# Kernel optimization log

Measured on AMD Instinct MI355X. Metric: run time of the kernel, lower is better.

Reference implementation:

```python
import jax, jax.numpy as jnp
import numpy as np

EMBED = 1024
HEADS = 16
HEAD_DIM = EMBED // HEADS
SCALE = HEAD_DIM ** -0.5


def setup_inputs() -> dict:
    key = jax.random.key(0)
    ks = jax.random.split(key, 5)
    B, N = 2, 2048
    x = jax.random.normal(ks[0], (B, N, EMBED), dtype=jnp.float32)
    # qkv Linear: weight [3*EMBED, EMBED], bias [3*EMBED]
    w_qkv = jax.random.normal(ks[1], (3 * EMBED, EMBED), dtype=jnp.float32) * (EMBED ** -0.5)
    b_qkv = jnp.zeros((3 * EMBED,), dtype=jnp.float32)
    # proj Linear: weight [EMBED, EMBED], bias [EMBED]
    w_proj = jax.random.normal(ks[2], (EMBED, EMBED), dtype=jnp.float32) * (EMBED ** -0.5)
    b_proj = jnp.zeros((EMBED,), dtype=jnp.float32)
    return {"x": x, "w_qkv": w_qkv, "b_qkv": b_qkv, "w_proj": w_proj, "b_proj": b_proj}


def reference(x, w_qkv, b_qkv, w_proj, b_proj):
    B, N, _ = x.shape
    # QKV projection: [B, N, 3*EMBED]
    qkv = jnp.einsum('bnc,dc->bnd', x, w_qkv) + b_qkv
    qkv = qkv.reshape(B, N, 3, HEADS, HEAD_DIM).transpose(2, 0, 3, 1, 4)  # [3, B, H, N, Dh]
    q, k, v = qkv[0], qkv[1], qkv[2]
    # Explicit attention: matmul -> scale -> softmax -> matmul (eval mode, no dropout)
    attn = jnp.einsum('bhqd,bhkd->bhqk', q, k) * SCALE
    attn = jax.nn.softmax(attn, axis=-1)
    out = jnp.einsum('bhqk,bhkd->bhqd', attn, v)
    out = out.transpose(0, 2, 1, 3).reshape(B, N, EMBED)
    # Output projection (gamma1 is Identity; dropouts are zero in eval)
    out = jnp.einsum('bnc,dc->bnd', out, w_proj) + b_proj
    return out
```

## Files before the change

kernel.cpp:

```cpp
#include <hip/hip_runtime.h>
#include <stdint.h>

#define SEQ 2048

typedef __attribute__((ext_vector_type(8))) short bf16x8;
typedef __attribute__((ext_vector_type(4))) float f32x4;
typedef __attribute__((ext_vector_type(4))) int i32x4;

typedef const __attribute__((address_space(1))) unsigned int GVT;
typedef __attribute__((address_space(3))) unsigned int LVT;

static __device__ __forceinline__ unsigned short f2bf(float f) {
  unsigned u = __builtin_bit_cast(unsigned, f);
  u += 0x7fffu + ((u >> 16) & 1u);
  return (unsigned short)(u >> 16);
}

static __device__ __forceinline__ unsigned pk_bf16(float lo, float hi) {
  unsigned r;
  asm("v_cvt_pk_bf16_f32 %0, %1, %2" : "=v"(r) : "v"(lo), "v"(hi));
  return r;
}

__global__ __launch_bounds__(256) void cvt3_kernel(
    const float* __restrict__ s0, unsigned short* __restrict__ d0, int n0,
    const float* __restrict__ s1, unsigned short* __restrict__ d1, int n1,
    const float* __restrict__ s2, unsigned short* __restrict__ d2, int n2) {
  int i = blockIdx.x * 256 + threadIdx.x;
  const int stride = gridDim.x * 256;
  const int total = n0 + n1 + n2;
  for (; i < total; i += stride) {
    const float* s;
    unsigned short* d;
    int k;
    if (i < n0) { s = s0; d = d0; k = i; }
    else if (i < n0 + n1) { s = s1; d = d1; k = i - n0; }
    else { s = s2; d = d2; k = i - n0 - n1; }
    float4 v = reinterpret_cast<const float4*>(s)[k];
    ushort4 o;
    o.x = f2bf(v.x); o.y = f2bf(v.y); o.z = f2bf(v.z); o.w = f2bf(v.w);
    reinterpret_cast<ushort4*>(d)[k] = o;
  }
}

__global__ __launch_bounds__(256, 3) void gemm_qkv_kernel(
    const unsigned short* __restrict__ A,
    const unsigned short* __restrict__ Bt,
    const float* __restrict__ bias,
    unsigned short* __restrict__ qb,
    unsigned short* __restrict__ kbuf,
    unsigned short* __restrict__ vtbuf) {
  __shared__ __align__(16) unsigned short As[2][128 * 32];
  __shared__ __align__(16) unsigned short Bs[2][128 * 32];
  const int tid = threadIdx.x;
  const int lane = tid & 63;
  const int wid = tid >> 6;
  const int wr = wid >> 1, wc = wid & 1;
  const int lin = blockIdx.y * 24 + blockIdx.x;
  const int wg = (lin & 7) * 96 + (lin >> 3);
  const int bm = wg / 24, bn = wg % 24;
  const int lr = lane & 15, hg = lane >> 4;

  f32x4 acc[4][4] = {};

  const int r0 = tid >> 2;
  const int c0 = (tid & 3) * 8;

  auto STAGE = [&](int b, int kt) {
    const unsigned short* ga0 = A + (size_t)(bm * 128 + r0) * 1024 + kt * 32 + c0;
    const unsigned short* ga1 = A + (size_t)(bm * 128 + r0 + 64) * 1024 + kt * 32 + c0;
    const unsigned short* gb0 = Bt + (size_t)(bn * 128 + r0) * 1024 + kt * 32 + c0;
    const unsigned short* gb1 = Bt + (size_t)(bn * 128 + r0 + 64) * 1024 + kt * 32 + c0;
    __builtin_amdgcn_global_load_lds((GVT*)ga0, (LVT*)&As[b][tid * 8], 16, 0, 0);
    __builtin_amdgcn_global_load_lds((GVT*)ga1, (LVT*)&As[b][(tid + 256) * 8], 16, 0, 0);
    __builtin_amdgcn_global_load_lds((GVT*)gb0, (LVT*)&Bs[b][tid * 8], 16, 0, 0);
    __builtin_amdgcn_global_load_lds((GVT*)gb1, (LVT*)&Bs[b][(tid + 256) * 8], 16, 0, 0);
  };

  STAGE(0, 0);
  int cur = 0;
  for (int kt = 0; kt < 32; ++kt) {
    __syncthreads();
    if (kt + 1 < 32) STAGE(cur ^ 1, kt + 1);
    bf16x8 af[4], bfr[4];
#pragma unroll
    for (int i = 0; i < 4; ++i) {
      af[i] = *reinterpret_cast<const bf16x8*>(&As[cur][(wr * 64 + i * 16 + lr) * 32 + hg * 8]);
      bfr[i] = *reinterpret_cast<const bf16x8*>(&Bs[cur][(wc * 64 + i * 16 + lr) * 32 + hg * 8]);
    }
    __builtin_amdgcn_s_setprio(1);
#pragma unroll
    for (int i = 0; i < 4; ++i)
#pragma unroll
      for (int j = 0; j < 4; ++j)
        acc[i][j] = __builtin_amdgcn_mfma_f32_16x16x32_bf16(af[i], bfr[j], acc[i][j], 0, 0, 0);
    __builtin_amdgcn_s_setprio(0);
    cur ^= 1;
  }

#pragma unroll
  for (int j = 0; j < 4; ++j) {
    const int col = bn * 128 + wc * 64 + j * 16 + lr;
    const float bv = bias[col];
    const int which = col >> 10;
    const int hh = (col >> 6) & 15;
    const int dh = col & 63;
    const float scl = which == 0 ? 0.18033688011112042f : 1.0f;
#pragma unroll
    for (int i = 0; i < 4; ++i) {
      if (which == 2) {
        const int row0 = bm * 128 + wr * 64 + i * 16 + hg * 4;
        const int b = row0 >> 11, n0 = row0 & 2047;
        ushort4 vv;
        vv.x = f2bf(acc[i][j][0] + bv);
        vv.y = f2bf(acc[i][j][1] + bv);
        vv.z = f2bf(acc[i][j][2] + bv);
        vv.w = f2bf(acc[i][j][3] + bv);
        *reinterpret_cast<ushort4*>(
            &vtbuf[((size_t)((b * 16 + hh) * 64 + dh)) * 2048 + n0]) = vv;
      } else {
        unsigned short* dst = which == 0 ? qb : kbuf;
#pragma unroll
        for (int r = 0; r < 4; ++r) {
          const int row = bm * 128 + wr * 64 + i * 16 + hg * 4 + r;
          const int b = row >> 11, n = row & 2047;
          dst[((size_t)((b * 16 + hh) * 2048 + n)) * 64 + dh] = f2bf((acc[i][j][r] + bv) * scl);
        }
      }
    }
  }
}

__global__ __launch_bounds__(256, 4) void gemm_proj_kernel(
    const unsigned short* __restrict__ A,
    const unsigned short* __restrict__ Bt,
    const float* __restrict__ bias,
    float* __restrict__ out) {
  __shared__ __align__(16) unsigned short As[2][32 * 32];
  __shared__ __align__(16) unsigned short Bs[2][128 * 32];
  const int tid = threadIdx.x;
  const int lane = tid & 63;
  const int wc = tid >> 6;
  const int lin = blockIdx.y * 8 + blockIdx.x;
  const int wg = (lin & 7) * 128 + (lin >> 3);
  const int bm = wg >> 3, bn = wg & 7;
  const int lr = lane & 15, hg = lane >> 4;

  f32x4 acc[2][2] = {};
  const int r0 = tid >> 2;
  const int c0 = (tid & 3) * 8;

  auto STAGE = [&](int b, int kt) {
    if (tid < 128) {
      const unsigned short* ga0 = A + (size_t)(bm * 32 + r0) * 1024 + kt * 32 + c0;
      __builtin_amdgcn_global_load_lds((GVT*)ga0, (LVT*)&As[b][tid * 8], 16, 0, 0);
    }
    const unsigned short* gb0 = Bt + (size_t)(bn * 128 + r0) * 1024 + kt * 32 + c0;
    const unsigned short* gb1 = Bt + (size_t)(bn * 128 + r0 + 64) * 1024 + kt * 32 + c0;
    __builtin_amdgcn_global_load_lds((GVT*)gb0, (LVT*)&Bs[b][tid * 8], 16, 0, 0);
    __builtin_amdgcn_global_load_lds((GVT*)gb1, (LVT*)&Bs[b][(tid + 256) * 8], 16, 0, 0);
  };

  STAGE(0, 0);
  int cur = 0;
  for (int kt = 0; kt < 32; ++kt) {
    __syncthreads();
    if (kt + 1 < 32) STAGE(cur ^ 1, kt + 1);
    bf16x8 af[2], bfr[2];
#pragma unroll
    for (int i = 0; i < 2; ++i)
      af[i] = *reinterpret_cast<const bf16x8*>(&As[cur][(i * 16 + lr) * 32 + hg * 8]);
#pragma unroll
    for (int j = 0; j < 2; ++j)
      bfr[j] = *reinterpret_cast<const bf16x8*>(&Bs[cur][(wc * 32 + j * 16 + lr) * 32 + hg * 8]);
    __builtin_amdgcn_s_setprio(1);
#pragma unroll
    for (int i = 0; i < 2; ++i)
#pragma unroll
      for (int j = 0; j < 2; ++j)
        acc[i][j] = __builtin_amdgcn_mfma_f32_16x16x32_bf16(af[i], bfr[j], acc[i][j], 0, 0, 0);
    __builtin_amdgcn_s_setprio(0);
    cur ^= 1;
  }

#pragma unroll
  for (int j = 0; j < 2; ++j) {
    const int col = bn * 128 + wc * 32 + j * 16 + lr;
    const float bv = bias[col];
#pragma unroll
    for (int i = 0; i < 2; ++i)
#pragma unroll
      for (int r = 0; r < 4; ++r) {
        const int row = bm * 32 + i * 16 + hg * 4 + r;
        out[(size_t)row * 1024 + col] = acc[i][j][r] + bv;
      }
  }
}

__global__ __launch_bounds__(512, 4) void attn_kernel(
    const unsigned short* __restrict__ qb,
    const unsigned short* __restrict__ kbuf,
    const unsigned short* __restrict__ vt,
    unsigned short* __restrict__ ao) {
  __shared__ __align__(16) unsigned short KVbuf[2][2][2][4096];
  const int tid = threadIdx.x;
  const int lane = tid & 63;
  const int wid = tid >> 6;
  const int ws = wid >> 2;
  const int wq = wid & 3;
  const int lr = lane & 15;
  const int hg = lane >> 4;
  const int lin = blockIdx.y * 16 + blockIdx.x;
  const int wg = (lin & 7) * 64 + (lin >> 3);
  const int qt = wg & 15;
  const int bh = wg >> 4;
  const size_t hbase = (size_t)bh * SEQ * 64;

  bf16x8 qf[2][2];
#pragma unroll
  for (int m = 0; m < 2; ++m) {
    const unsigned short* qp =
        qb + hbase + (size_t)(qt * 128 + wq * 32 + m * 16 + lr) * 64 + hg * 8;
    qf[m][0] = *reinterpret_cast<const bf16x8*>(qp);
    qf[m][1] = *reinterpret_cast<const bf16x8*>(qp + 32);
  }

  f32x4 accO[2][4] = {};
  float l_run[2] = {0.0f, 0.0f};

  const int srow = tid >> 3;
  const int ssw = ((tid & 7) ^ (srow & 7)) * 8;
  auto STAGE = [&](int b, int kt) {
#pragma unroll
    for (int s = 0; s < 2; ++s) {
      const unsigned short* gk =
          kbuf + hbase + (size_t)(s * 1024 + kt * 64 + srow) * 64 + ssw;
      __builtin_amdgcn_global_load_lds((GVT*)gk, (LVT*)&KVbuf[0][s][b][tid * 8], 16, 0, 0);
      const unsigned short* gv =
          vt + hbase + (size_t)srow * 2048 + s * 1024 + kt * 64 + ssw;
      __builtin_amdgcn_global_load_lds((GVT*)gv, (LVT*)&KVbuf[1][s][b][tid * 8], 16, 0, 0);
    }
  };

  STAGE(0, 0);
  int cur = 0;
  const int sw0 = (hg ^ (lr & 7)) * 8;
  const int sw1 = ((hg + 4) ^ (lr & 7)) * 8;

  for (int kt = 0; kt < 16; ++kt) {
    __syncthreads();
    if (kt + 1 < 16) STAGE(cur ^ 1, kt + 1);

    const unsigned short* Ksb = &KVbuf[0][ws][cur][0];
    const unsigned short* Vsb = &KVbuf[1][ws][cur][0];

    f32x4 accT[2][4] = {};
    __builtin_amdgcn_s_setprio(1);
#pragma unroll
    for (int j = 0; j < 4; ++j) {
      const bf16x8 kf0 = *reinterpret_cast<const bf16x8*>(&Ksb[(j * 16 + lr) * 64 + sw0]);
      const bf16x8 kf1 = *reinterpret_cast<const bf16x8*>(&Ksb[(j * 16 + lr) * 64 + sw1]);
      accT[0][j] = __builtin_amdgcn_mfma_f32_16x16x32_bf16(kf0, qf[0][0], accT[0][j], 0, 0, 0);
      accT[0][j] = __builtin_amdgcn_mfma_f32_16x16x32_bf16(kf1, qf[0][1], accT[0][j], 0, 0, 0);
      accT[1][j] = __builtin_amdgcn_mfma_f32_16x16x32_bf16(kf0, qf[1][0], accT[1][j], 0, 0, 0);
      accT[1][j] = __builtin_amdgcn_mfma_f32_16x16x32_bf16(kf1, qf[1][1], accT[1][j], 0, 0, 0);
    }
    __builtin_amdgcn_s_setprio(0);

    bf16x8 pB[2][2];
#pragma unroll
    for (int m = 0; m < 2; ++m) {
      unsigned w[4][2];
      float ps0 = 0.f, ps1 = 0.f;
#pragma unroll
      for (int j = 0; j < 4; ++j) {
        const float p0 = __builtin_amdgcn_exp2f(accT[m][j][0]);
        const float p1 = __builtin_amdgcn_exp2f(accT[m][j][1]);
        const float p2 = __builtin_amdgcn_exp2f(accT[m][j][2]);
        const float p3 = __builtin_amdgcn_exp2f(accT[m][j][3]);
        ps0 += (p0 + p1);
        ps1 += (p2 + p3);
        w[j][0] = pk_bf16(p0, p1);
        w[j][1] = pk_bf16(p2, p3);
      }
      l_run[m] += ps0 + ps1;
#pragma unroll
      for (int h = 0; h < 2; ++h) {
        unsigned e0 = w[2 * h][0], e1 = w[2 * h][1];
        unsigned f0 = w[2 * h + 1][0], f1 = w[2 * h + 1][1];
        asm("v_permlane32_swap_b32 %0, %1" : "+v"(e0), "+v"(f0));
        asm("v_permlane32_swap_b32 %0, %1" : "+v"(e1), "+v"(f1));
        asm("v_permlane16_swap_b32 %0, %1" : "+v"(e0), "+v"(f0));
        asm("v_permlane16_swap_b32 %0, %1" : "+v"(e1), "+v"(f1));
        const i32x4 pw = {(int)e0, (int)e1, (int)f0, (int)f1};
        pB[m][h] = __builtin_bit_cast(bf16x8, pw);
      }
    }

    __builtin_amdgcn_s_setprio(1);
#pragma unroll
    for (int jd = 0; jd < 4; ++jd) {
      const bf16x8 v0 = *reinterpret_cast<const bf16x8*>(&Vsb[(jd * 16 + lr) * 64 + sw0]);
      const bf16x8 v1 = *reinterpret_cast<const bf16x8*>(&Vsb[(jd * 16 + lr) * 64 + sw1]);
      accO[0][jd] = __builtin_amdgcn_mfma_f32_16x16x32_bf16(v0, pB[0][0], accO[0][jd], 0, 0, 0);
      accO[0][jd] = __builtin_amdgcn_mfma_f32_16x16x32_bf16(v1, pB[0][1], accO[0][jd], 0, 0, 0);
      accO[1][jd] = __builtin_amdgcn_mfma_f32_16x16x32_bf16(v0, pB[1][0], accO[1][jd], 0, 0, 0);
      accO[1][jd] = __builtin_amdgcn_mfma_f32_16x16x32_bf16(v1, pB[1][1], accO[1][jd], 0, 0, 0);
    }
    __builtin_amdgcn_s_setprio(0);
    cur ^= 1;
  }

#pragma unroll
  for (int m = 0; m < 2; ++m) {
    l_run[m] += __shfl_xor(l_run[m], 16);
    l_run[m] += __shfl_xor(l_run[m], 32);
  }

  float* scr = (float*)&KVbuf[0][0][0][0];
  const int sbase = (wq * 64 + lane) * 37;
  __syncthreads();
  if (ws == 1) {
#pragma unroll
    for (int m = 0; m < 2; ++m) {
#pragma unroll
      for (int jd = 0; jd < 4; ++jd)
#pragma unroll
        for (int r = 0; r < 4; ++r) scr[sbase + m * 16 + jd * 4 + r] = accO[m][jd][r];
      scr[sbase + 32 + m] = l_run[m];
    }
  }
  __syncthreads();
  if (ws == 0) {
    const int b = bh >> 4, hh = bh & 15;
#pragma unroll
    for (int m = 0; m < 2; ++m) {
      const float inv = 1.0f / (l_run[m] + scr[sbase + 32 + m]);
      const int qrow = qt * 128 + wq * 32 + m * 16 + lr;
      unsigned short* dst = ao + (size_t)(b * 2048 + qrow) * 1024 + hh * 64;
#pragma unroll
      for (int jd = 0; jd < 4; ++jd) {
        const float o0 = (accO[m][jd][0] + scr[sbase + m * 16 + jd * 4 + 0]) * inv;
        const float o1 = (accO[m][jd][1] + scr[sbase + m * 16 + jd * 4 + 1]) * inv;
        const float o2 = (accO[m][jd][2] + scr[sbase + m * 16 + jd * 4 + 2]) * inv;
        const float o3 = (accO[m][jd][3] + scr[sbase + m * 16 + jd * 4 + 3]) * inv;
        uint2 o;
        o.x = pk_bf16(o0, o1);
        o.y = pk_bf16(o2, o3);
        *reinterpret_cast<uint2*>(dst + jd * 16 + hg * 4) = o;
      }
    }
  }
}

extern "C" void kernel_launch(void* const* d_in, const int* in_sizes, int n_in,
                              void* d_out, int out_size, void* d_ws, size_t ws_size,
                              hipStream_t stream) {
  const float* x = (const float*)d_in[0];
  const float* w_qkv = (const float*)d_in[1];
  const float* b_qkv = (const float*)d_in[2];
  const float* w_proj = (const float*)d_in[3];
  const float* b_proj = (const float*)d_in[4];
  float* out = (float*)d_out;
  char* ws = (char*)d_ws;
  unsigned short* x_bf = (unsigned short*)(ws);
  unsigned short* ao_bf = (unsigned short*)(ws);
  unsigned short* wq_bf = (unsigned short*)(ws + (8ull << 20));
  unsigned short* wp_bf = (unsigned short*)(ws + (14ull << 20));
  unsigned short* q_bf = (unsigned short*)(ws + (16ull << 20));
  unsigned short* k_bf = (unsigned short*)(ws + (24ull << 20));
  unsigned short* vt_bf = (unsigned short*)(ws + (32ull << 20));

  cvt3_kernel<<<2048, 256, 0, stream>>>(x, x_bf, 4096 * 1024 / 4,
                                        w_qkv, wq_bf, 3072 * 1024 / 4,
                                        w_proj, wp_bf, 1024 * 1024 / 4);
  gemm_qkv_kernel<<<dim3(24, 32), 256, 0, stream>>>(x_bf, wq_bf, b_qkv, q_bf, k_bf, vt_bf);
  attn_kernel<<<dim3(16, 32), 512, 0, stream>>>(q_bf, k_bf, vt_bf, ao_bf);
  gemm_proj_kernel<<<dim3(8, 128), 256, 0, stream>>>(ao_bf, wp_bf, b_proj, out);
}
```

Baseline: 112.1 us.

## Halve attention K/V tile per stage and shrink LDS to raise occupancy

Shrinks the attention kernel's shared K/V staging buffer from 64 KB to 32 KB by moving 32 keys per stage (two halves of 32 for each split warp group) instead of 64. The K-loop now runs twice as many iterations. Per-iteration register state is also smaller (accT 2x2, one P fragment). The launch bound goes from 4 to 6 waves per SIMD. The epilogue merge now reuses a smaller scratch area, reducing per m-half with extra barriers. The aim is more resident workgroups to hide latency, at the cost of twice as many barriers and staging rounds, plus smaller MFMA batches between syncs.

Result: slower. 117.3 us (+4.7%).

```diff
diff --git a/kernel.cpp b/kernel.cpp
--- a/kernel.cpp
+++ b/kernel.cpp
@@ -197,12 +197,12 @@
   }
 }
 
-__global__ __launch_bounds__(512, 4) void attn_kernel(
+__global__ __launch_bounds__(512, 6) void attn_kernel(
     const unsigned short* __restrict__ qb,
     const unsigned short* __restrict__ kbuf,
     const unsigned short* __restrict__ vt,
     unsigned short* __restrict__ ao) {
-  __shared__ __align__(16) unsigned short KVbuf[2][2][2][4096];
+  __shared__ __align__(16) unsigned short SMEM[16384];
   const int tid = threadIdx.x;
   const int lane = tid & 63;
   const int wid = tid >> 6;
@@ -229,16 +229,19 @@
   float l_run[2] = {0.0f, 0.0f};
 
   const int srow = tid >> 3;
-  const int ssw = ((tid & 7) ^ (srow & 7)) * 8;
+  const int sc8 = tid & 7;
   auto STAGE = [&](int b, int kt) {
-#pragma unroll
-    for (int s = 0; s < 2; ++s) {
-      const unsigned short* gk =
-          kbuf + hbase + (size_t)(s * 1024 + kt * 64 + srow) * 64 + ssw;
-      __builtin_amdgcn_global_load_lds((GVT*)gk, (LVT*)&KVbuf[0][s][b][tid * 8], 16, 0, 0);
-      const unsigned short* gv =
-          vt + hbase + (size_t)srow * 2048 + s * 1024 + kt * 64 + ssw;
-      __builtin_amdgcn_global_load_lds((GVT*)gv, (LVT*)&KVbuf[1][s][b][tid * 8], 16, 0, 0);
+    {
+      const int ksrc = sc8 ^ (srow & 7);
+      const unsigned short* gk = kbuf + hbase +
+          (size_t)(((srow >> 5) * 1024) + kt * 32 + (srow & 31)) * 64 + ksrc * 8;
+      __builtin_amdgcn_global_load_lds((GVT*)gk, (LVT*)&SMEM[b * 4096 + tid * 8], 16, 0, 0);
+    }
+    {
+      const int ce = sc8 ^ (srow & 7);
+      const unsigned short* gv = vt + hbase + (size_t)srow * 2048 +
+          (ce >> 2) * 1024 + kt * 32 + (ce & 3) * 8;
+      __builtin_amdgcn_global_load_lds((GVT*)gv, (LVT*)&SMEM[8192 + b * 4096 + tid * 8], 16, 0, 0);
     }
   };
 
@@ -246,20 +249,22 @@
   int cur = 0;
   const int sw0 = (hg ^ (lr & 7)) * 8;
   const int sw1 = ((hg + 4) ^ (lr & 7)) * 8;
-
-  for (int kt = 0; kt < 16; ++kt) {
-    __syncthreads();
-    if (kt + 1 < 16) STAGE(cur ^ 1, kt + 1);
-
-    const unsigned short* Ksb = &KVbuf[0][ws][cur][0];
-    const unsigned short* Vsb = &KVbuf[1][ws][cur][0];
-
-    f32x4 accT[2][4] = {};
+  const int swv = ((ws * 4 + hg) ^ (lr & 7)) * 8;
+
+  for (int kt = 0; kt < 32; ++kt) {
+    __syncthreads();
+    if (kt + 1 < 32) STAGE(cur ^ 1, kt + 1);
+
+    const unsigned short* Ksb = &SMEM[cur * 4096];
+    const unsigned short* Vsb = &SMEM[8192 + cur * 4096];
+
+    f32x4 accT[2][2] = {};
     __builtin_amdgcn_s_setprio(1);
 #pragma unroll
-    for (int j = 0; j < 4; ++j) {
-      const bf16x8 kf0 = *reinterpret_cast<const bf16x8*>(&Ksb[(j * 16 + lr) * 64 + sw0]);
-      const bf16x8 kf1 = *reinterpret_cast<const bf16x8*>(&Ksb[(j * 16 + lr) * 64 + sw1]);
+    for (int j = 0; j < 2; ++j) {
+      const int krow = ws * 32 + j * 16 + lr;
+      const bf16x8 kf0 = *reinterpret_cast<const bf16x8*>(&Ksb[krow * 64 + sw0]);
+      const bf16x8 kf1 = *reinterpret_cast<const bf16x8*>(&Ksb[krow * 64 + sw1]);
       accT[0][j] = __builtin_amdgcn_mfma_f32_16x16x32_bf16(kf0, qf[0][0], accT[0][j], 0, 0, 0);
       accT[0][j] = __builtin_amdgcn_mfma_f32_16x16x32_bf16(kf1, qf[0][1], accT[0][j], 0, 0, 0);
       accT[1][j] = __builtin_amdgcn_mfma_f32_16x16x32_bf16(kf0, qf[1][0], accT[1][j], 0, 0, 0);
@@ -267,45 +272,34 @@
     }
     __builtin_amdgcn_s_setprio(0);
 
-    bf16x8 pB[2][2];
+    bf16x8 pB[2];
 #pragma unroll
     for (int m = 0; m < 2; ++m) {
-      unsigned w[4][2];
-      float ps0 = 0.f, ps1 = 0.f;
-#pragma unroll
-      for (int j = 0; j < 4; ++j) {
-        const float p0 = __builtin_amdgcn_exp2f(accT[m][j][0]);
-        const float p1 = __builtin_amdgcn_exp2f(accT[m][j][1]);
-        const float p2 = __builtin_amdgcn_exp2f(accT[m][j][2]);
-        const float p3 = __builtin_amdgcn_exp2f(accT[m][j][3]);
-        ps0 += (p0 + p1);
-        ps1 += (p2 + p3);
-        w[j][0] = pk_bf16(p0, p1);
-        w[j][1] = pk_bf16(p2, p3);
-      }
-      l_run[m] += ps0 + ps1;
-#pragma unroll
-      for (int h = 0; h < 2; ++h) {
-        unsigned e0 = w[2 * h][0], e1 = w[2 * h][1];
-        unsigned f0 = w[2 * h + 1][0], f1 = w[2 * h + 1][1];
-        asm("v_permlane32_swap_b32 %0, %1" : "+v"(e0), "+v"(f0));
-        asm("v_permlane32_swap_b32 %0, %1" : "+v"(e1), "+v"(f1));
-        asm("v_permlane16_swap_b32 %0, %1" : "+v"(e0), "+v"(f0));
-        asm("v_permlane16_swap_b32 %0, %1" : "+v"(e1), "+v"(f1));
-        const i32x4 pw = {(int)e0, (int)e1, (int)f0, (int)f1};
-        pB[m][h] = __builtin_bit_cast(bf16x8, pw);
-      }
+      const float p0 = __builtin_amdgcn_exp2f(accT[m][0][0]);
+      const float p1 = __builtin_amdgcn_exp2f(accT[m][0][1]);
+      const float p2 = __builtin_amdgcn_exp2f(accT[m][0][2]);
+      const float p3 = __builtin_amdgcn_exp2f(accT[m][0][3]);
+      const float p4 = __builtin_amdgcn_exp2f(accT[m][1][0]);
+      const float p5 = __builtin_amdgcn_exp2f(accT[m][1][1]);
+      const float p6 = __builtin_amdgcn_exp2f(accT[m][1][2]);
+      const float p7 = __builtin_amdgcn_exp2f(accT[m][1][3]);
+      l_run[m] += ((p0 + p1) + (p2 + p3)) + ((p4 + p5) + (p6 + p7));
+      unsigned e0 = pk_bf16(p0, p1), e1 = pk_bf16(p2, p3);
+      unsigned f0 = pk_bf16(p4, p5), f1 = pk_bf16(p6, p7);
+      asm("v_permlane32_swap_b32 %0, %1" : "+v"(e0), "+v"(f0));
+      asm("v_permlane32_swap_b32 %0, %1" : "+v"(e1), "+v"(f1));
+      asm("v_permlane16_swap_b32 %0, %1" : "+v"(e0), "+v"(f0));
+      asm("v_permlane16_swap_b32 %0, %1" : "+v"(e1), "+v"(f1));
+      const i32x4 pw = {(int)e0, (int)e1, (int)f0, (int)f1};
+      pB[m] = __builtin_bit_cast(bf16x8, pw);
     }
 
     __builtin_amdgcn_s_setprio(1);
 #pragma unroll
     for (int jd = 0; jd < 4; ++jd) {
-      const bf16x8 v0 = *reinterpret_cast<const bf16x8*>(&Vsb[(jd * 16 + lr) * 64 + sw0]);
-      const bf16x8 v1 = *reinterpret_cast<const bf16x8*>(&Vsb[(jd * 16 + lr) * 64 + sw1]);
-      accO[0][jd] = __builtin_amdgcn_mfma_f32_16x16x32_bf16(v0, pB[0][0], accO[0][jd], 0, 0, 0);
-      accO[0][jd] = __builtin_amdgcn_mfma_f32_16x16x32_bf16(v1, pB[0][1], accO[0][jd], 0, 0, 0);
-      accO[1][jd] = __builtin_amdgcn_mfma_f32_16x16x32_bf16(v0, pB[1][0], accO[1][jd], 0, 0, 0);
-      accO[1][jd] = __builtin_amdgcn_mfma_f32_16x16x32_bf16(v1, pB[1][1], accO[1][jd], 0, 0, 0);
+      const bf16x8 vfr = *reinterpret_cast<const bf16x8*>(&Vsb[(jd * 16 + lr) * 64 + swv]);
+      accO[0][jd] = __builtin_amdgcn_mfma_f32_16x16x32_bf16(vfr, pB[0], accO[0][jd], 0, 0, 0);
+      accO[1][jd] = __builtin_amdgcn_mfma_f32_16x16x32_bf16(vfr, pB[1], accO[1][jd], 0, 0, 0);
     }
     __builtin_amdgcn_s_setprio(0);
     cur ^= 1;
@@ -317,33 +311,30 @@
     l_run[m] += __shfl_xor(l_run[m], 32);
   }
 
-  float* scr = (float*)&KVbuf[0][0][0][0];
-  const int sbase = (wq * 64 + lane) * 37;
-  __syncthreads();
-  if (ws == 1) {
-#pragma unroll
-    for (int m = 0; m < 2; ++m) {
+  float* scr = (float*)&SMEM[0];
+  const int sbase = (wq * 64 + lane) * 17;
+  const int b = bh >> 4, hh = bh & 15;
+#pragma unroll
+  for (int m = 0; m < 2; ++m) {
+    __syncthreads();
+    if (ws == 1) {
 #pragma unroll
       for (int jd = 0; jd < 4; ++jd)
 #pragma unroll
-        for (int r = 0; r < 4; ++r) scr[sbase + m * 16 + jd * 4 + r] = accO[m][jd][r];
-      scr[sbase + 32 + m] = l_run[m];
-    }
-  }
-  __syncthreads();
-  if (ws == 0) {
-    const int b = bh >> 4, hh = bh & 15;
-#pragma unroll
-    for (int m = 0; m < 2; ++m) {
-      const float inv = 1.0f / (l_run[m] + scr[sbase + 32 + m]);
+        for (int r = 0; r < 4; ++r) scr[sbase + jd * 4 + r] = accO[m][jd][r];
+      scr[sbase + 16] = l_run[m];
+    }
+    __syncthreads();
+    if (ws == 0) {
+      const float inv = 1.0f / (l_run[m] + scr[sbase + 16]);
       const int qrow = qt * 128 + wq * 32 + m * 16 + lr;
       unsigned short* dst = ao + (size_t)(b * 2048 + qrow) * 1024 + hh * 64;
 #pragma unroll
       for (int jd = 0; jd < 4; ++jd) {
-        const float o0 = (accO[m][jd][0] + scr[sbase + m * 16 + jd * 4 + 0]) * inv;
-        const float o1 = (accO[m][jd][1] + scr[sbase + m * 16 + jd * 4 + 1]) * inv;
-        const float o2 = (accO[m][jd][2] + scr[sbase + m * 16 + jd * 4 + 2]) * inv;
-        const float o3 = (accO[m][jd][3] + scr[sbase + m * 16 + jd * 4 + 3]) * inv;
+        const float o0 = (accO[m][jd][0] + scr[sbase + jd * 4 + 0]) * inv;
+        const float o1 = (accO[m][jd][1] + scr[sbase + jd * 4 + 1]) * inv;
+        const float o2 = (accO[m][jd][2] + scr[sbase + jd * 4 + 2]) * inv;
+        const float o3 = (accO[m][jd][3] + scr[sbase + jd * 4 + 3]) * inv;
         uint2 o;
         o.x = pk_bf16(o0, o1);
         o.y = pk_bf16(o2, o3);
```
